# Kernel tuning notes

Hardware: AMD Instinct MI355X
Metric: run time of the kernel (lower is better)

The kernel has to match this reference:

```python
import jax, jax.numpy as jnp
import numpy as np

B, N_PTS, M_ROIS = 2, 8192, 2048
C_IN, O, H, NS = 128, 256, 4, 32
RADIUS = 1.6
BN_EPS = 1e-5
SCALE = 10.0  # point cloud extent


def setup_inputs() -> dict:
    key = jax.random.key(0)
    ks = jax.random.split(key, 20)
    f32 = jnp.float32
    Cg = C_IN + 3  # grouper concats relative xyz to features

    def kaiming(k, shape, fan_in):
        return jax.random.normal(k, shape, f32) * np.sqrt(2.0 / fan_in)

    inp = {
        "xyz": jax.random.uniform(ks[0], (B, N_PTS, 3), f32) * SCALE,
        "new_xyz": jax.random.uniform(ks[1], (B, M_ROIS, 3), f32) * SCALE,
        "features": jax.random.normal(ks[2], (B, C_IN, N_PTS), f32),
        # conv1d (kernel=1, no bias) weights, torch layout (out, in)
        "pos_w": kaiming(ks[3], (O, 3), 3),
        "key_w": kaiming(ks[4], (O, Cg), Cg),
        "val_w1": kaiming(ks[5], (O, Cg), Cg),
        "bn1_g": jnp.ones((O,), f32), "bn1_b": jnp.zeros((O,), f32),
        "val_w2": kaiming(ks[6], (O, O), O),
        "bn2_g": jnp.ones((O,), f32), "bn2_b": jnp.zeros((O,), f32),
        "attn_w": kaiming(ks[7], (H, O), O),
        # sigmoid-gated coefficient linears (no bias)
        "kc_w": kaiming(ks[8], (O, O), O),
        "qc_w": kaiming(ks[9], (O, O), O),
        "qkc_w": kaiming(ks[10], (O, O), O),
        "vc_w": kaiming(ks[11], (O, O), O),
        # cls/reg weight MLPs: Linear(O,O//2)+ReLU, Linear(O//2,1)+Sigmoid
        "cls_w1": kaiming(ks[12], (O // 2, O), O), "cls_b1": jnp.zeros((O // 2,), f32),
        "cls_w2": kaiming(ks[13], (1, O // 2), O // 2), "cls_b2": jnp.zeros((1,), f32),
        "reg_w1": kaiming(ks[14], (O // 2, O), O), "reg_b1": jnp.zeros((O // 2,), f32),
        "reg_w2": kaiming(ks[15], (1, O // 2), O // 2), "reg_b2": jnp.zeros((1,), f32),
    }
    return inp


def _bn(x, g, b):
    # eval-mode BatchNorm1d with running_mean=0, running_var=1 (init state)
    return g[None, :, None] * (x * (1.0 / np.sqrt(1.0 + BN_EPS))) + b[None, :, None]


def _conv1x1(w, x):  # (O,C) x (M,C,NS) -> (M,O,NS)
    return jnp.einsum('oc,mcn->mon', w, x)


def _ball_group(pts, q):
    # ball query: first NS points within RADIUS of each query (pad with first hit)
    n_tot = pts.shape[0]
    d2 = jnp.sum((q[:, None, :] - pts[None, :, :]) ** 2, axis=-1)  # (M, Ntot)
    order = jnp.where(d2 < RADIUS ** 2, jnp.arange(n_tot, dtype=jnp.int32), n_tot)
    neg_vals, idx = jax.lax.top_k(-order, NS)  # smallest indices among in-ball pts
    valid = (-neg_vals) < n_tot
    idx = jnp.where(valid, idx, idx[:, :1])  # pad with first neighbor
    has_any = valid[:, :1]
    idx = jnp.where(has_any, idx, 0)  # empty balls -> point 0
    return idx, ~has_any[:, 0]


def reference(xyz, new_xyz, features, pos_w, key_w, val_w1, bn1_g, bn1_b,
              val_w2, bn2_g, bn2_b, attn_w, kc_w, qc_w, qkc_w, vc_w,
              cls_w1, cls_b1, cls_w2, cls_b2, reg_w1, reg_b1, reg_w2, reg_b2):
    pts = xyz.reshape(-1, 3)                                   # (Ntot, 3)
    feats = features.transpose(0, 2, 1).reshape(-1, C_IN)      # (Ntot, C)
    q = new_xyz.reshape(-1, 3)                                 # (M, 3)

    idx, empty_mask = _ball_group(pts, q)                      # (M, NS)
    gx = pts[idx] - q[:, None, :]                              # relative xyz (M,NS,3)
    gxt = gx.transpose(0, 2, 1)                                # (M,3,NS)
    gf = jnp.concatenate([gx, feats[idx]], axis=-1).transpose(0, 2, 1)  # (M,C+3,NS)

    pos = jax.nn.relu(_conv1x1(pos_w, gxt))                    # (M,O,NS)
    key = jax.nn.relu(_conv1x1(key_w, gf))                     # (M,O,NS)
    v = jax.nn.relu(_bn(_conv1x1(val_w1, gf), bn1_g, bn1_b))
    val = jax.nn.relu(_bn(_conv1x1(val_w2, v), bn2_g, bn2_b))  # (M,O,NS)
    pos_key = pos * key

    sig = jax.nn.sigmoid
    v_c = sig(pos.mean(2) @ vc_w.T)                            # (M,O)
    q_c = sig(pos.mean(2) @ qc_w.T)
    k_c = sig(key.mean(2) @ kc_w.T)
    qk_c = sig(pos_key.mean(2) @ qkc_w.T)

    val = val + pos * v_c[:, :, None]
    attn_emb = pos * q_c[:, :, None] + key * k_c[:, :, None] + pos_key * qk_c[:, :, None]
    attn = jax.nn.softmax(jnp.einsum('ho,mon->mhn', attn_w, attn_emb), axis=-1)  # (M,H,NS)

    m = val.shape[0]
    vh = val.reshape(m, H, O // H, NS)
    new_features = jnp.einsum('mhdn,mhn->mhd', vh, attn).reshape(m, O)  # (M,O)

    def gate(x, w1, b1, w2, b2):
        return sig(jax.nn.relu(x @ w1.T + b1) @ w2.T + b2)

    cls_features = new_features * gate(new_features, cls_w1, cls_b1, cls_w2, cls_b2)
    reg_features = new_features * gate(new_features, reg_w1, reg_b1, reg_w2, reg_b2)
    return new_features, cls_features, reg_features
```

## Files before the change

### kernel.cpp

```cpp
#include <hip/hip_runtime.h>

#define DI __device__ __forceinline__

typedef __attribute__((ext_vector_type(8))) short bf16x8;
typedef __attribute__((ext_vector_type(4))) short s16x4;
typedef __attribute__((ext_vector_type(4))) float f32x4;
typedef __attribute__((ext_vector_type(2))) unsigned int u32x2;

DI short f2bs(float x){ unsigned u = __float_as_uint(x);
  return (short)((u + 0x7FFF + ((u >> 16) & 1)) >> 16); }
DI float bs2f(short s){ return __uint_as_float(((unsigned)(unsigned short)s) << 16); }
DI unsigned pack2(float a, float b){
  return (unsigned)(unsigned short)f2bs(a) | ((unsigned)(unsigned short)f2bs(b) << 16);
}
DI f32x4 MFMA(bf16x8 a, bf16x8 b, f32x4 c){
  return __builtin_amdgcn_mfma_f32_16x16x32_bf16(a, b, c, 0, 0, 0);
}

constexpr int NP   = 8192;
constexpr int NTOT = 16384;
constexpr int M    = 4096;
constexpr int C    = 128;
constexpr int O    = 256;
constexpr int NS   = 32;
constexpr int H    = 4;
constexpr int KP   = 160;
constexpr int GFS  = 168;
constexpr int VS   = 264;
constexpr float BNS = 0.99999500003749969f;

__global__ __launch_bounds__(256) void k_transpose(const float* __restrict__ feat,
                                                   short* __restrict__ fT){
  __shared__ float tile[128][65];
  int blk = blockIdx.x;
  int b  = blk >> 7;
  int n0 = (blk & 127) << 6;
  int t = threadIdx.x;
  int nn = t & 63, c4 = t >> 6;
  const float* src = feat + (size_t)b * C * NP;
  for(int i = 0; i < 32; i++){
    int c = c4 * 32 + i;
    tile[c][nn] = src[(size_t)c * NP + n0 + nn];
  }
  __syncthreads();
  int c2 = t & 127, nb = t >> 7;
  for(int j = 0; j < 32; j++){
    int n = nb + j * 2;
    fT[((size_t)(b * NP + n0 + n)) * C + c2] = f2bs(tile[c2][n]);
  }
}

__global__ __launch_bounds__(256) void k_pack(
    const float* __restrict__ kw, const float* __restrict__ v1w,
    const float* __restrict__ v2w,
    const float* __restrict__ vcw, const float* __restrict__ qcw,
    const float* __restrict__ kcw, const float* __restrict__ qkcw,
    const float* __restrict__ cw1, const float* __restrict__ rw1,
    short* __restrict__ keyP, short* __restrict__ v1P,
    short* __restrict__ v2b,
    short* __restrict__ gw,
    short* __restrict__ cw1b, short* __restrict__ rw1b)
{
  int i = blockIdx.x * 256 + threadIdx.x;
  if(i < O * KP){
    int o = i / KP, k = i % KP;
    float a = 0.0f, b = 0.0f;
    if(k < 128){ a = kw[o*131 + 3 + k]; b = v1w[o*131 + 3 + k]; }
    else if(k < 131){ a = kw[o*131 + (k - 128)]; b = v1w[o*131 + (k - 128)]; }
    keyP[i] = f2bs(a);
    v1P[i]  = f2bs(b);
  }
  if(i < O * O){
    v2b[i] = f2bs(v2w[i]);
    gw[0*O*O + i] = f2bs(vcw[i]);
    gw[1*O*O + i] = f2bs(qcw[i]);
    gw[2*O*O + i] = f2bs(kcw[i]);
    gw[3*O*O + i] = f2bs(qkcw[i]);
  }
  if(i < (O/2) * O){
    cw1b[i] = f2bs(cw1[i]);
    rw1b[i] = f2bs(rw1[i]);
  }
}

__global__ __launch_bounds__(64) void k_ballq(const float* __restrict__ xyz,
                                              const float* __restrict__ nxyz,
                                              int* __restrict__ idxo,
                                              float* __restrict__ gxo){
#pragma clang fp contract(off)
  int m = blockIdx.x;
  int lane = threadIdx.x;
  float qx = nxyz[m*3+0], qy = nxyz[m*3+1], qz = nxyz[m*3+2];
  __shared__ int sel[NS];
  int cnt = 0;
  for(int base = 0; base < NTOT; base += 64){
    int p = base + lane;
    float dx = qx - xyz[p*3+0], dy = qy - xyz[p*3+1], dz = qz - xyz[p*3+2];
    float d2 = dx*dx + dy*dy;
    d2 = d2 + dz*dz;
    bool pred = d2 < 2.56f;
    unsigned long long bal = __ballot(pred);
    if(pred){
      int pos = cnt + __popcll(bal & ((1ull << lane) - 1ull));
      if(pos < NS) sel[pos] = p;
    }
    cnt += __popcll(bal);
    if(cnt >= NS) break;
  }
  __syncthreads();
  if(lane < NS){
    int s = 0;
    if(cnt > 0) s = (lane < cnt) ? sel[lane] : sel[0];
    idxo[m*NS + lane] = s;
    gxo[(m*NS+lane)*3+0] = xyz[s*3+0] - qx;
    gxo[(m*NS+lane)*3+1] = xyz[s*3+1] - qy;
    gxo[(m*NS+lane)*3+2] = xyz[s*3+2] - qz;
  }
}

__global__ __launch_bounds__(256, 2) void k_conv(
    const short* __restrict__ fT,
    const short* __restrict__ keyP, const short* __restrict__ v1P,
    const short* __restrict__ v2b,
    const float* __restrict__ posw,
    const float* __restrict__ g1, const float* __restrict__ b1,
    const float* __restrict__ g2, const float* __restrict__ b2,
    const int* __restrict__ idxw, const float* __restrict__ gxw,
    short* __restrict__ keyo, short* __restrict__ valo,
    float* __restrict__ mPos, float* __restrict__ mKey, float* __restrict__ mPK,
    int q0)
{
  int lq2 = blockIdx.x, t = threadIdx.x;
  int w = t >> 6, l = t & 63;
  int col = l & 15, kq = l >> 4;
  int ro = w * 64;
  __shared__ __align__(16) short gf[64 * GFS];
  __shared__ __align__(16) short vst[64 * VS];
  __shared__ float gxs[64 * 4];
  __shared__ int  sel[64];
  int qg0 = q0 + lq2 * 2;
  if(t < 64){
    int qi = t >> 5, n = t & 31;
    int gq = qg0 + qi;
    sel[t] = idxw[gq*NS + n];
    gxs[t*4+0] = gxw[(gq*NS+n)*3+0];
    gxs[t*4+1] = gxw[(gq*NS+n)*3+1];
    gxs[t*4+2] = gxw[(gq*NS+n)*3+2];
    gxs[t*4+3] = 0.0f;
  }
  __syncthreads();
  for(int i = 0; i < 16; i++){
    int n = w*16 + i;
    int p = sel[n];
    *(unsigned*)&gf[n*GFS + l*2] = *(const unsigned*)(fT + (size_t)p * C + l*2);
  }
  {
    int n = t & 63, j0 = (t >> 6) * 8;
    for(int j = 0; j < 8; j++){
      int k = j0 + j;
      float v = (k < 3) ? gxs[n*4 + k] : 0.0f;
      gf[n*GFS + 128 + k] = f2bs(v);
    }
  }
  __syncthreads();

  f32x4 acc[4][4];
  const f32x4 vzero = {0.0f, 0.0f, 0.0f, 0.0f};

  for(int mt=0;mt<4;mt++) for(int nt=0;nt<4;nt++) acc[mt][nt] = vzero;
  for(int ks = 0; ks < 5; ks++){
    bf16x8 bf[4];
    for(int nt=0;nt<4;nt++)
      bf[nt] = *(const bf16x8*)&gf[(nt*16+col)*GFS + ks*32 + kq*8];
    for(int mt = 0; mt < 4; mt++){
      bf16x8 a = *(const bf16x8*)(v1P + (size_t)(ro + mt*16 + col)*KP + ks*32 + kq*8);
      for(int nt=0;nt<4;nt++) acc[mt][nt] = MFMA(a, bf[nt], acc[mt][nt]);
    }
  }
  for(int mt=0;mt<4;mt++){
    int o0 = ro + mt*16 + kq*4;
    float gg[4], bb[4];
    for(int r=0;r<4;r++){ gg[r] = g1[o0+r]; bb[r] = b1[o0+r]; }
    for(int nt=0;nt<4;nt++){
      s16x4 pk;
      for(int r=0;r<4;r++)
        pk[r] = f2bs(fmaxf(gg[r]*(acc[mt][nt][r] * BNS) + bb[r], 0.0f));
      *(s16x4*)&vst[(nt*16+col)*VS + o0] = pk;
    }
  }

  for(int mt=0;mt<4;mt++) for(int nt=0;nt<4;nt++) acc[mt][nt] = vzero;
  for(int ks = 0; ks < 5; ks++){
    bf16x8 bf[4];
    for(int nt=0;nt<4;nt++)
      bf[nt] = *(const bf16x8*)&gf[(nt*16+col)*GFS + ks*32 + kq*8];
    for(int mt = 0; mt < 4; mt++){
      bf16x8 a = *(const bf16x8*)(keyP + (size_t)(ro + mt*16 + col)*KP + ks*32 + kq*8);
      for(int nt=0;nt<4;nt++) acc[mt][nt] = MFMA(a, bf[nt], acc[mt][nt]);
    }
  }
  for(int mt=0;mt<4;mt++){
    int o0 = ro + mt*16 + kq*4;
    float pw[4][3];
    for(int r=0;r<4;r++){ pw[r][0]=posw[(o0+r)*3+0]; pw[r][1]=posw[(o0+r)*3+1];
                          pw[r][2]=posw[(o0+r)*3+2]; }
    for(int qi=0; qi<2; qi++){
      float sp[4]={0,0,0,0}, sk[4]={0,0,0,0}, spk[4]={0,0,0,0};
      for(int h=0; h<2; h++){
        int nt = qi*2 + h;
        int n  = nt*16 + col;
        float gx0 = gxs[n*4+0], gx1 = gxs[n*4+1], gx2 = gxs[n*4+2];
        float kvv[4];
        for(int r=0;r<4;r++){
          float kk = fmaxf(acc[mt][nt][r], 0.0f);
          kvv[r] = kk;
          float pv = fmaxf(pw[r][0]*gx0 + pw[r][1]*gx1 + pw[r][2]*gx2, 0.0f);
          sp[r] += pv; sk[r] += kk; spk[r] += pv*kk;
        }
        int lql = lq2*2 + qi;
        int nn = h*16 + col;
        u32x2 pk2 = { pack2(kvv[0], kvv[1]), pack2(kvv[2], kvv[3]) };
        *(u32x2*)&keyo[((size_t)lql*NS + nn)*O + o0] = pk2;
      }
      for(int r=0;r<4;r++){
        float a = sp[r], b = sk[r], c = spk[r];
        for(int msk=1; msk<16; msk<<=1){
          a += __shfl_xor(a, msk); b += __shfl_xor(b, msk); c += __shfl_xor(c, msk);
        }
        if(col == 0){
          int lql = lq2*2 + qi;
          mPos[(size_t)lql*O + o0 + r] = a * 0.03125f;
          mKey[(size_t)lql*O + o0 + r] = b * 0.03125f;
          mPK [(size_t)lql*O + o0 + r] = c * 0.03125f;
        }
      }
    }
  }
  __syncthreads();

  for(int mt=0;mt<4;mt++) for(int nt=0;nt<4;nt++) acc[mt][nt] = vzero;
  for(int ks = 0; ks < 8; ks++){
    bf16x8 bf[4];
    for(int nt=0;nt<4;nt++)
      bf[nt] = *(const bf16x8*)&vst[(nt*16+col)*VS + ks*32 + kq*8];
    for(int mt = 0; mt < 4; mt++){
      bf16x8 a = *(const bf16x8*)(v2b + (size_t)(ro + mt*16 + col)*O + ks*32 + kq*8);
      for(int nt=0;nt<4;nt++) acc[mt][nt] = MFMA(a, bf[nt], acc[mt][nt]);
    }
  }
  for(int mt=0;mt<4;mt++){
    int o0 = ro + mt*16 + kq*4;
    float gg[4], bb[4];
    for(int r=0;r<4;r++){ gg[r] = g2[o0+r]; bb[r] = b2[o0+r]; }
    for(int nt=0;nt<4;nt++){
      float vv[4];
      for(int r=0;r<4;r++)
        vv[r] = fmaxf(gg[r]*(acc[mt][nt][r] * BNS) + bb[r], 0.0f);
      int lql = lq2*2 + (nt>>1);
      int nn  = (nt&1)*16 + col;
      u32x2 pk2 = { pack2(vv[0], vv[1]), pack2(vv[2], vv[3]) };
      *(u32x2*)&valo[((size_t)lql*NS + nn)*O + o0] = pk2;
    }
  }
}

__global__ __launch_bounds__(256) void k_gates(
    const float* __restrict__ mPos, const float* __restrict__ mKey,
    const float* __restrict__ mPK, const short* __restrict__ gw,
    float* __restrict__ gates)
{
  int t = threadIdx.x, w = t >> 6, l = t & 63, col = l & 15, kq = l >> 4;
  int lq0 = blockIdx.x * 16;
  const float* A  = (w < 2) ? mPos : ((w == 2) ? mKey : mPK);
  const short* Wg = gw + (size_t)w * O * O;
  f32x4 acc[16];
  const f32x4 vzero = {0.0f,0.0f,0.0f,0.0f};
  for(int i=0;i<16;i++) acc[i] = vzero;
  for(int ks = 0; ks < 8; ks++){
    union { bf16x8 v; short e[8]; } u;
    const float* ap = A + (size_t)(lq0 + col)*O + ks*32 + kq*8;
    for(int j = 0; j < 8; j++) u.e[j] = f2bs(ap[j]);
    for(int nt = 0; nt < 16; nt++){
      bf16x8 bv = *(const bf16x8*)(Wg + (size_t)(nt*16 + col)*O + ks*32 + kq*8);
      acc[nt] = MFMA(u.v, bv, acc[nt]);
    }
  }
  for(int nt=0;nt<16;nt++) for(int r=0;r<4;r++){
    int lqq = lq0 + kq*4 + r;
    int oo = nt*16 + col;
    gates[((size_t)lqq*4 + w)*O + oo] = 1.0f / (1.0f + expf(-acc[nt][r]));
  }
}

__global__ __launch_bounds__(256) void k_attn(
    const short* __restrict__ keyw, const short* __restrict__ valw,
    const float* __restrict__ gxw, const float* __restrict__ posw,
    const float* __restrict__ attw, const float* __restrict__ gates,
    float* __restrict__ outNF, int q0)
{
  int lq = blockIdx.x, q = q0 + lq, t = threadIdx.x;
  __shared__ float emL[O * 33];
  __shared__ float attnL[H * NS];
  __shared__ float gxs[NS * 3];
  __shared__ float partial[256];
  if(t < 96) gxs[t] = gxw[q*96 + t];
  float vc  = gates[((size_t)lq*4 + 0)*O + t];
  float qc  = gates[((size_t)lq*4 + 1)*O + t];
  float kc  = gates[((size_t)lq*4 + 2)*O + t];
  float qkc = gates[((size_t)lq*4 + 3)*O + t];
  float pw0 = posw[t*3+0], pw1 = posw[t*3+1], pw2 = posw[t*3+2];
  __syncthreads();
  float posr[NS];
  for(int n = 0; n < NS; n++)
    posr[n] = fmaxf(pw0*gxs[n*3] + pw1*gxs[n*3+1] + pw2*gxs[n*3+2], 0.0f);
  for(int n = 0; n < NS; n++){
    float k = bs2f(keyw[((size_t)lq*NS + n)*O + t]);
    emL[t*33 + n] = posr[n]*qc + k*kc + posr[n]*k*qkc;
  }
  __syncthreads();
  {
    int idx = t & 127, h = idx >> 5, n = idx & 31, half = t >> 7;
    float s = 0;
    const float* aw = attw + h*O + half*128;
    for(int o = 0; o < 128; o++) s += aw[o] * emL[(half*128 + o)*33 + n];
    partial[t] = s;
  }
  __syncthreads();
  if(t < 128){
    int h = t >> 5, n = t & 31;
    float s = partial[t] + partial[t + 128];
    float mx = s;
    for(int msk=1; msk<32; msk<<=1) mx = fmaxf(mx, __shfl_xor(mx, msk));
    float e = expf(s - mx);
    float sum = e;
    for(int msk=1; msk<32; msk<<=1) sum += __shfl_xor(sum, msk);
    attnL[h*NS + n] = e / sum;
  }
  __syncthreads();
  int h = t >> 6;
  float nf = 0;
  for(int n = 0; n < NS; n++){
    float v = bs2f(valw[((size_t)lq*NS + n)*O + t]);
    nf += (v + posr[n]*vc) * attnL[h*NS + n];
  }
  outNF[(size_t)q*O + t] = nf;
}

__global__ __launch_bounds__(256) void k_fgate(
    const float* __restrict__ nf,
    const short* __restrict__ cw1b, const float* __restrict__ cb1,
    const float* __restrict__ cw2, const float* __restrict__ cb2,
    const short* __restrict__ rw1b, const float* __restrict__ rb1,
    const float* __restrict__ rw2, const float* __restrict__ rb2,
    float* __restrict__ outC, float* __restrict__ outR)
{
  int t = threadIdx.x, w = t >> 6, l = t & 63, col = l & 15, kq = l >> 4;
  int q0 = blockIdx.x * 64;
  __shared__ float sC[64], sR[64];
  f32x4 acc[16];
  const f32x4 vzero = {0.0f,0.0f,0.0f,0.0f};
  for(int i=0;i<16;i++) acc[i] = vzero;
  int arow = q0 + w*16 + col;
  for(int ks = 0; ks < 8; ks++){
    union { bf16x8 v; short e[8]; } u;
    const float* ap = nf + (size_t)arow*O + ks*32 + kq*8;
    for(int j = 0; j < 8; j++) u.e[j] = f2bs(ap[j]);
    for(int nt = 0; nt < 16; nt++){
      const short* W1 = (nt < 8) ? cw1b : rw1b;
      int j = (nt & 7)*16 + col;
      bf16x8 bv = *(const bf16x8*)(W1 + (size_t)j*O + ks*32 + kq*8);
      acc[nt] = MFMA(u.v, bv, acc[nt]);
    }
  }
  for(int r = 0; r < 4; r++){
    float pc = 0, pr = 0;
    for(int nt = 0; nt < 8; nt++){
      int j = nt*16 + col;
      pc += fmaxf(acc[nt][r] + cb1[j], 0.0f) * cw2[j];
    }
    for(int nt = 8; nt < 16; nt++){
      int j = (nt - 8)*16 + col;
      pr += fmaxf(acc[nt][r] + rb1[j], 0.0f) * rw2[j];
    }
    for(int msk=1; msk<16; msk<<=1){ pc += __shfl_xor(pc, msk); pr += __shfl_xor(pr, msk); }
    if(col == 0){
      int qq = w*16 + kq*4 + r;
      sC[qq] = 1.0f / (1.0f + expf(-(pc + cb2[0])));
      sR[qq] = 1.0f / (1.0f + expf(-(pr + rb2[0])));
    }
  }
  __syncthreads();
  for(int qq = 0; qq < 64; qq++){
    float nv = nf[(size_t)(q0 + qq)*O + t];
    outC[(size_t)(q0 + qq)*O + t] = nv * sC[qq];
    outR[(size_t)(q0 + qq)*O + t] = nv * sR[qq];
  }
}

extern "C" void kernel_launch(void* const* d_in, const int* in_sizes, int n_in,
                              void* d_out, int out_size, void* d_ws, size_t ws_size,
                              hipStream_t stream)
{
  const float* xyz  = (const float*)d_in[0];
  const float* nxyz = (const float*)d_in[1];
  const float* feat = (const float*)d_in[2];
  const float* posw = (const float*)d_in[3];
  const float* keyw = (const float*)d_in[4];
  const float* v1w  = (const float*)d_in[5];
  const float* bn1g = (const float*)d_in[6];
  const float* bn1b = (const float*)d_in[7];
  const float* v2w  = (const float*)d_in[8];
  const float* bn2g = (const float*)d_in[9];
  const float* bn2b = (const float*)d_in[10];
  const float* attw = (const float*)d_in[11];
  const float* kcw  = (const float*)d_in[12];
  const float* qcw  = (const float*)d_in[13];
  const float* qkcw = (const float*)d_in[14];
  const float* vcw  = (const float*)d_in[15];
  const float* cw1  = (const float*)d_in[16];
  const float* cb1  = (const float*)d_in[17];
  const float* cw2  = (const float*)d_in[18];
  const float* cb2  = (const float*)d_in[19];
  const float* rw1  = (const float*)d_in[20];
  const float* rb1  = (const float*)d_in[21];
  const float* rw2  = (const float*)d_in[22];
  const float* rb2  = (const float*)d_in[23];

  const size_t fixedB = 12000000;
  const size_t perQ   = 40960;
  int Q = 64;
  for(int cand : {4096, 2048, 1024, 512, 256, 128}){
    if(fixedB + (size_t)cand*perQ <= ws_size){ Q = cand; break; }
  }

  char* p = (char*)d_ws;
  auto alloc = [&](size_t bytes){ char* r = p; p += (bytes + 255) & ~size_t(255); return r; };
  short* fT    = (short*)alloc((size_t)NTOT*C*2);
  short* keyP  = (short*)alloc((size_t)O*KP*2);
  short* v1P   = (short*)alloc((size_t)O*KP*2);
  short* v2b   = (short*)alloc((size_t)O*O*2);
  short* gw    = (short*)alloc((size_t)4*O*O*2);
  short* cw1b  = (short*)alloc((size_t)(O/2)*O*2);
  short* rw1b  = (short*)alloc((size_t)(O/2)*O*2);
  int*   idxw  = (int*)  alloc((size_t)M*NS*4);
  float* gxw   = (float*)alloc((size_t)M*NS*3*4);
  short* keyo  = (short*)alloc((size_t)Q*NS*O*2);
  short* valo  = (short*)alloc((size_t)Q*NS*O*2);
  float* mPos  = (float*)alloc((size_t)Q*O*4);
  float* mKey  = (float*)alloc((size_t)Q*O*4);
  float* mPK   = (float*)alloc((size_t)Q*O*4);
  float* gates = (float*)alloc((size_t)Q*4*O*4);

  float* outNF = (float*)d_out;
  float* outC  = outNF + (size_t)M*O;
  float* outR  = outC  + (size_t)M*O;

  k_transpose<<<256, 256, 0, stream>>>(feat, fT);
  k_pack     <<<256, 256, 0, stream>>>(keyw, v1w, v2w, vcw, qcw, kcw, qkcw, cw1, rw1,
                                       keyP, v1P, v2b, gw, cw1b, rw1b);
  k_ballq    <<<M,   64,  0, stream>>>(xyz, nxyz, idxw, gxw);
  for(int q0 = 0; q0 < M; q0 += Q){
    k_conv  <<<Q/2,  256, 0, stream>>>(fT, keyP, v1P, v2b,
                                       posw, bn1g, bn1b, bn2g, bn2b,
                                       idxw, gxw, keyo, valo, mPos, mKey, mPK, q0);
    k_gates <<<Q/16, 256, 0, stream>>>(mPos, mKey, mPK, gw, gates);
    k_attn  <<<Q,    256, 0, stream>>>(keyo, valo, gxw, posw, attw, gates, outNF, q0);
  }
  k_fgate   <<<M/64, 256, 0, stream>>>(outNF, cw1b, cb1, cw2, cb2, rw1b, rb1, rw2, rb2, outC, outR);
}
```

Baseline: 409.1 us.

## Split xyz term out of conv GEMMs and stage outputs through LDS for coalesced stores

The 3 relative-xyz input channels are taken out of the padded K=160 GEMMs and added as an fp32 rank-3 FMA in the epilogue, so the key and val1 convolutions need 4 MFMA k-steps instead of 5. The gf LDS tile shrinks and occupancy is raised to 3 blocks per CU. The key and val outputs are staged in LDS and written to global memory with wide 16-byte row copies instead of scattered 8-byte stores. This adds extra barriers and some epilogue math, and the xyz contribution is now computed in fp32 rather than bf16, which slightly changes numerics.

Result: slower. 438.1 us (+7.1%).

```diff
diff --git a/kernel.cpp b/kernel.cpp
--- a/kernel.cpp
+++ b/kernel.cpp
@@ -5,14 +5,10 @@
 typedef __attribute__((ext_vector_type(8))) short bf16x8;
 typedef __attribute__((ext_vector_type(4))) short s16x4;
 typedef __attribute__((ext_vector_type(4))) float f32x4;
-typedef __attribute__((ext_vector_type(2))) unsigned int u32x2;
 
 DI short f2bs(float x){ unsigned u = __float_as_uint(x);
   return (short)((u + 0x7FFF + ((u >> 16) & 1)) >> 16); }
 DI float bs2f(short s){ return __uint_as_float(((unsigned)(unsigned short)s) << 16); }
-DI unsigned pack2(float a, float b){
-  return (unsigned)(unsigned short)f2bs(a) | ((unsigned)(unsigned short)f2bs(b) << 16);
-}
 DI f32x4 MFMA(bf16x8 a, bf16x8 b, f32x4 c){
   return __builtin_amdgcn_mfma_f32_16x16x32_bf16(a, b, c, 0, 0, 0);
 }
@@ -24,10 +20,18 @@
 constexpr int O    = 256;
 constexpr int NS   = 32;
 constexpr int H    = 4;
-constexpr int KP   = 160;
-constexpr int GFS  = 168;
+constexpr int GFS  = 136;
 constexpr int VS   = 264;
 constexpr float BNS = 0.99999500003749969f;
+
+DI void copy64(short* __restrict__ dst, const short* __restrict__ src, int t){
+  int row = t >> 2, off = (t & 3) * 64;
+  const short* sp = src + row*VS + off;
+  short* dp = dst + (size_t)row*O + off;
+  #pragma unroll
+  for(int j = 0; j < 8; j++)
+    *(bf16x8*)(dp + j*8) = *(const bf16x8*)(sp + j*8);
+}
 
 __global__ __launch_bounds__(256) void k_transpose(const float* __restrict__ feat,
                                                    short* __restrict__ fT){
@@ -52,23 +56,29 @@
 
 __global__ __launch_bounds__(256) void k_pack(
     const float* __restrict__ kw, const float* __restrict__ v1w,
-    const float* __restrict__ v2w,
+    const float* __restrict__ v2w, const float* __restrict__ pw,
     const float* __restrict__ vcw, const float* __restrict__ qcw,
     const float* __restrict__ kcw, const float* __restrict__ qkcw,
     const float* __restrict__ cw1, const float* __restrict__ rw1,
     short* __restrict__ keyP, short* __restrict__ v1P,
+    float* __restrict__ kgx, float* __restrict__ v1gx, float* __restrict__ pgx,
     short* __restrict__ v2b,
     short* __restrict__ gw,
     short* __restrict__ cw1b, short* __restrict__ rw1b)
 {
   int i = blockIdx.x * 256 + threadIdx.x;
-  if(i < O * KP){
-    int o = i / KP, k = i % KP;
-    float a = 0.0f, b = 0.0f;
-    if(k < 128){ a = kw[o*131 + 3 + k]; b = v1w[o*131 + 3 + k]; }
-    else if(k < 131){ a = kw[o*131 + (k - 128)]; b = v1w[o*131 + (k - 128)]; }
-    keyP[i] = f2bs(a);
-    v1P[i]  = f2bs(b);
+  if(i < O * C){
+    int o = i >> 7, k = i & 127;
+    keyP[i] = f2bs(kw[o*131 + 3 + k]);
+    v1P[i]  = f2bs(v1w[o*131 + 3 + k]);
+  }
+  if(i < O){
+    for(int j = 0; j < 3; j++){
+      kgx [i*4+j] = kw [i*131 + j];
+      v1gx[i*4+j] = v1w[i*131 + j];
+      pgx [i*4+j] = pw [i*3 + j];
+    }
+    kgx[i*4+3] = 0.0f; v1gx[i*4+3] = 0.0f; pgx[i*4+3] = 0.0f;
   }
   if(i < O * O){
     v2b[i] = f2bs(v2w[i]);
@@ -118,11 +128,12 @@
   }
 }
 
-__global__ __launch_bounds__(256, 2) void k_conv(
+__global__ __launch_bounds__(256, 3) void k_conv(
     const short* __restrict__ fT,
     const short* __restrict__ keyP, const short* __restrict__ v1P,
+    const float* __restrict__ kgx, const float* __restrict__ v1gx,
+    const float* __restrict__ pgx,
     const short* __restrict__ v2b,
-    const float* __restrict__ posw,
     const float* __restrict__ g1, const float* __restrict__ b1,
     const float* __restrict__ g2, const float* __restrict__ b2,
     const int* __restrict__ idxw, const float* __restrict__ gxw,
@@ -154,73 +165,40 @@
     int p = sel[n];
     *(unsigned*)&gf[n*GFS + l*2] = *(const unsigned*)(fT + (size_t)p * C + l*2);
   }
-  {
-    int n = t & 63, j0 = (t >> 6) * 8;
-    for(int j = 0; j < 8; j++){
-      int k = j0 + j;
-      float v = (k < 3) ? gxs[n*4 + k] : 0.0f;
-      gf[n*GFS + 128 + k] = f2bs(v);
-    }
-  }
   __syncthreads();
 
   f32x4 acc[4][4];
   const f32x4 vzero = {0.0f, 0.0f, 0.0f, 0.0f};
 
   for(int mt=0;mt<4;mt++) for(int nt=0;nt<4;nt++) acc[mt][nt] = vzero;
-  for(int ks = 0; ks < 5; ks++){
+  for(int ks = 0; ks < 4; ks++){
     bf16x8 bf[4];
     for(int nt=0;nt<4;nt++)
       bf[nt] = *(const bf16x8*)&gf[(nt*16+col)*GFS + ks*32 + kq*8];
     for(int mt = 0; mt < 4; mt++){
-      bf16x8 a = *(const bf16x8*)(v1P + (size_t)(ro + mt*16 + col)*KP + ks*32 + kq*8);
+      bf16x8 a = *(const bf16x8*)(keyP + (size_t)(ro + mt*16 + col)*C + ks*32 + kq*8);
       for(int nt=0;nt<4;nt++) acc[mt][nt] = MFMA(a, bf[nt], acc[mt][nt]);
     }
   }
   for(int mt=0;mt<4;mt++){
     int o0 = ro + mt*16 + kq*4;
-    float gg[4], bb[4];
-    for(int r=0;r<4;r++){ gg[r] = g1[o0+r]; bb[r] = b1[o0+r]; }
-    for(int nt=0;nt<4;nt++){
-      s16x4 pk;
-      for(int r=0;r<4;r++)
-        pk[r] = f2bs(fmaxf(gg[r]*(acc[mt][nt][r] * BNS) + bb[r], 0.0f));
-      *(s16x4*)&vst[(nt*16+col)*VS + o0] = pk;
-    }
-  }
-
-  for(int mt=0;mt<4;mt++) for(int nt=0;nt<4;nt++) acc[mt][nt] = vzero;
-  for(int ks = 0; ks < 5; ks++){
-    bf16x8 bf[4];
-    for(int nt=0;nt<4;nt++)
-      bf[nt] = *(const bf16x8*)&gf[(nt*16+col)*GFS + ks*32 + kq*8];
-    for(int mt = 0; mt < 4; mt++){
-      bf16x8 a = *(const bf16x8*)(keyP + (size_t)(ro + mt*16 + col)*KP + ks*32 + kq*8);
-      for(int nt=0;nt<4;nt++) acc[mt][nt] = MFMA(a, bf[nt], acc[mt][nt]);
-    }
-  }
-  for(int mt=0;mt<4;mt++){
-    int o0 = ro + mt*16 + kq*4;
-    float pw[4][3];
-    for(int r=0;r<4;r++){ pw[r][0]=posw[(o0+r)*3+0]; pw[r][1]=posw[(o0+r)*3+1];
-                          pw[r][2]=posw[(o0+r)*3+2]; }
+    f32x4 kg[4], pg[4];
+    for(int r=0;r<4;r++){ kg[r] = *(const f32x4*)(kgx + (o0+r)*4);
+                          pg[r] = *(const f32x4*)(pgx + (o0+r)*4); }
     for(int qi=0; qi<2; qi++){
       float sp[4]={0,0,0,0}, sk[4]={0,0,0,0}, spk[4]={0,0,0,0};
       for(int h=0; h<2; h++){
         int nt = qi*2 + h;
         int n  = nt*16 + col;
         float gx0 = gxs[n*4+0], gx1 = gxs[n*4+1], gx2 = gxs[n*4+2];
-        float kvv[4];
+        s16x4 pk;
         for(int r=0;r<4;r++){
-          float kk = fmaxf(acc[mt][nt][r], 0.0f);
-          kvv[r] = kk;
-          float pv = fmaxf(pw[r][0]*gx0 + pw[r][1]*gx1 + pw[r][2]*gx2, 0.0f);
+          float kk = fmaxf(acc[mt][nt][r] + kg[r][0]*gx0 + kg[r][1]*gx1 + kg[r][2]*gx2, 0.0f);
+          float pv = fmaxf(pg[r][0]*gx0 + pg[r][1]*gx1 + pg[r][2]*gx2, 0.0f);
+          pk[r] = f2bs(kk);
           sp[r] += pv; sk[r] += kk; spk[r] += pv*kk;
         }
-        int lql = lq2*2 + qi;
-        int nn = h*16 + col;
-        u32x2 pk2 = { pack2(kvv[0], kvv[1]), pack2(kvv[2], kvv[3]) };
-        *(u32x2*)&keyo[((size_t)lql*NS + nn)*O + o0] = pk2;
+        *(s16x4*)&vst[n*VS + o0] = pk;
       }
       for(int r=0;r<4;r++){
         float a = sp[r], b = sk[r], c = spk[r];
@@ -237,6 +215,37 @@
     }
   }
   __syncthreads();
+  copy64(keyo + (size_t)lq2*64*O, vst, t);
+
+  for(int mt=0;mt<4;mt++) for(int nt=0;nt<4;nt++) acc[mt][nt] = vzero;
+  for(int ks = 0; ks < 4; ks++){
+    bf16x8 bf[4];
+    for(int nt=0;nt<4;nt++)
+      bf[nt] = *(const bf16x8*)&gf[(nt*16+col)*GFS + ks*32 + kq*8];
+    for(int mt = 0; mt < 4; mt++){
+      bf16x8 a = *(const bf16x8*)(v1P + (size_t)(ro + mt*16 + col)*C + ks*32 + kq*8);
+      for(int nt=0;nt<4;nt++) acc[mt][nt] = MFMA(a, bf[nt], acc[mt][nt]);
+    }
+  }
+  __syncthreads();
+  for(int mt=0;mt<4;mt++){
+    int o0 = ro + mt*16 + kq*4;
+    f32x4 vg[4];
+    float gg[4], bb[4];
+    for(int r=0;r<4;r++){ vg[r] = *(const f32x4*)(v1gx + (o0+r)*4);
+                          gg[r] = g1[o0+r]; bb[r] = b1[o0+r]; }
+    for(int nt=0;nt<4;nt++){
+      int n = nt*16 + col;
+      float gx0 = gxs[n*4+0], gx1 = gxs[n*4+1], gx2 = gxs[n*4+2];
+      s16x4 pk;
+      for(int r=0;r<4;r++){
+        float x = acc[mt][nt][r] + vg[r][0]*gx0 + vg[r][1]*gx1 + vg[r][2]*gx2;
+        pk[r] = f2bs(fmaxf(gg[r]*(x * BNS) + bb[r], 0.0f));
+      }
+      *(s16x4*)&vst[n*VS + o0] = pk;
+    }
+  }
+  __syncthreads();
 
   for(int mt=0;mt<4;mt++) for(int nt=0;nt<4;nt++) acc[mt][nt] = vzero;
   for(int ks = 0; ks < 8; ks++){
@@ -248,20 +257,22 @@
       for(int nt=0;nt<4;nt++) acc[mt][nt] = MFMA(a, bf[nt], acc[mt][nt]);
     }
   }
+  s16x4 valS[4][4];
   for(int mt=0;mt<4;mt++){
     int o0 = ro + mt*16 + kq*4;
     float gg[4], bb[4];
     for(int r=0;r<4;r++){ gg[r] = g2[o0+r]; bb[r] = b2[o0+r]; }
-    for(int nt=0;nt<4;nt++){
-      float vv[4];
+    for(int nt=0;nt<4;nt++)
       for(int r=0;r<4;r++)
-        vv[r] = fmaxf(gg[r]*(acc[mt][nt][r] * BNS) + bb[r], 0.0f);
-      int lql = lq2*2 + (nt>>1);
-      int nn  = (nt&1)*16 + col;
-      u32x2 pk2 = { pack2(vv[0], vv[1]), pack2(vv[2], vv[3]) };
-      *(u32x2*)&valo[((size_t)lql*NS + nn)*O + o0] = pk2;
-    }
-  }
+        valS[mt][nt][r] = f2bs(fmaxf(gg[r]*(acc[mt][nt][r] * BNS) + bb[r], 0.0f));
+  }
+  __syncthreads();
+  for(int mt=0;mt<4;mt++) for(int nt=0;nt<4;nt++){
+    int n = nt*16 + col;
+    *(s16x4*)&vst[n*VS + ro + mt*16 + kq*4] = valS[mt][nt];
+  }
+  __syncthreads();
+  copy64(valo + (size_t)lq2*64*O, vst, t);
 }
 
 __global__ __launch_bounds__(256) void k_gates(
@@ -436,8 +447,11 @@
   char* p = (char*)d_ws;
   auto alloc = [&](size_t bytes){ char* r = p; p += (bytes + 255) & ~size_t(255); return r; };
   short* fT    = (short*)alloc((size_t)NTOT*C*2);
-  short* keyP  = (short*)alloc((size_t)O*KP*2);
-  short* v1P   = (short*)alloc((size_t)O*KP*2);
+  short* keyP  = (short*)alloc((size_t)O*C*2);
+  short* v1P   = (short*)alloc((size_t)O*C*2);
+  float* kgx   = (float*)alloc((size_t)O*4*4);
+  float* v1gx  = (float*)alloc((size_t)O*4*4);
+  float* pgx   = (float*)alloc((size_t)O*4*4);
   short* v2b   = (short*)alloc((size_t)O*O*2);
   short* gw    = (short*)alloc((size_t)4*O*O*2);
   short* cw1b  = (short*)alloc((size_t)(O/2)*O*2);
@@ -456,12 +470,12 @@
   float* outR  = outC  + (size_t)M*O;
 
   k_transpose<<<256, 256, 0, stream>>>(feat, fT);
-  k_pack     <<<256, 256, 0, stream>>>(keyw, v1w, v2w, vcw, qcw, kcw, qkcw, cw1, rw1,
-                                       keyP, v1P, v2b, gw, cw1b, rw1b);
+  k_pack     <<<256, 256, 0, stream>>>(keyw, v1w, v2w, posw, vcw, qcw, kcw, qkcw, cw1, rw1,
+                                       keyP, v1P, kgx, v1gx, pgx, v2b, gw, cw1b, rw1b);
   k_ballq    <<<M,   64,  0, stream>>>(xyz, nxyz, idxw, gxw);
   for(int q0 = 0; q0 < M; q0 += Q){
-    k_conv  <<<Q/2,  256, 0, stream>>>(fT, keyP, v1P, v2b,
-                                       posw, bn1g, bn1b, bn2g, bn2b,
+    k_conv  <<<Q/2,  256, 0, stream>>>(fT, keyP, v1P, kgx, v1gx, pgx, v2b,
+                                       bn1g, bn1b, bn2g, bn2b,
                                        idxw, gxw, keyo, valo, mPos, mKey, mPK, q0);
     k_gates <<<Q/16, 256, 0, stream>>>(mPos, mKey, mPK, gw, gates);
     k_attn  <<<Q,    256, 0, stream>>>(keyo, valo, gxw, posw, attw, gates, outNF, q0);
```
